# Kernel optimization log

Hardware: AMD Instinct MI355X
Metric: run time of the kernel (lower is better)

## Reference

```python
import jax, jax.numpy as jnp
import numpy as np

DIM = 1024
NUM_EXPERTS = 8
TOP_K = 2
B, S = 2, 2048
HID = 4 * DIM


def setup_inputs() -> dict:
    key = jax.random.key(0)
    ks = jax.random.split(key, 7)
    scale = 0.02
    x = jax.random.normal(ks[0], (B, S, DIM), dtype=jnp.float32)
    gate_w = jax.random.normal(ks[1], (DIM, NUM_EXPERTS), dtype=jnp.float32) * scale
    gate_b = jnp.zeros((NUM_EXPERTS,), dtype=jnp.float32)
    w1 = jax.random.normal(ks[2], (NUM_EXPERTS, DIM, HID), dtype=jnp.float32) * scale
    b1 = jnp.zeros((NUM_EXPERTS, HID), dtype=jnp.float32)
    w2 = jax.random.normal(ks[3], (NUM_EXPERTS, HID, DIM), dtype=jnp.float32) * scale
    b2 = jnp.zeros((NUM_EXPERTS, DIM), dtype=jnp.float32)
    return {"x": x, "gate_w": gate_w, "gate_b": gate_b,
            "w1": w1, "b1": b1, "w2": w2, "b2": b2}


def reference(x, gate_w, gate_b, w1, b1, w2, b2):
    # Gate: [B,S,E]
    gates = jnp.einsum('bsd,de->bse', x, gate_w) + gate_b
    top_w, top_idx = jax.lax.top_k(gates, TOP_K)          # [B,S,K]
    probs = jax.nn.softmax(top_w, axis=-1)                # softmax over selected logits
    # Dense all-expert FFN (matches original: every expert runs on every token)
    h = jnp.einsum('bsd,edh->bseh', x, w1) + b1           # [B,S,E,4D]
    h = jax.nn.gelu(h, approximate=False)                 # exact GELU (torch default)
    y = jnp.einsum('bseh,ehd->bsed', h, w2) + b2          # [B,S,E,D]
    # Select top-k experts per token and combine
    sel = jnp.take_along_axis(y, top_idx[..., None], axis=2)   # [B,S,K,D]
    return jnp.sum(sel * probs[..., None], axis=2)        # [B,S,D]
```

## Files before the change

### kernel.cpp

```cpp
#include <hip/hip_runtime.h>
#include <hip/hip_bf16.h>

#define T_TOKENS 4096
#define DIM      1024
#define HID      4096
#define NE       8
#define CAP      4096
#define SPLITS   4
#define KSP      (HID / SPLITS)

typedef __attribute__((ext_vector_type(8))) short  bf16x8;
typedef __attribute__((ext_vector_type(4))) float  f32x4;
typedef __attribute__((ext_vector_type(4))) ushort u16x4;

__device__ static inline ushort f2bf(float f) {
    __hip_bfloat16 h = __float2bfloat16(f);
    return *(ushort*)&h;
}

__device__ static inline void gll16(const void* g, void* l) {
    __builtin_amdgcn_global_load_lds(
        (const __attribute__((address_space(1))) void*)g,
        (__attribute__((address_space(3))) void*)l,
        16, 0, 0);
}

#define MFMA16(a, b, c) __builtin_amdgcn_mfma_f32_16x16x32_bf16((a), (b), (c), 0, 0, 0)

__global__ __launch_bounds__(64) void gate_kernel(
    const float* __restrict__ x, const float* __restrict__ gw,
    const float* __restrict__ gb, __hip_bfloat16* __restrict__ xb,
    int* __restrict__ counts, int* __restrict__ tlist, float* __restrict__ plist)
{
    const int tok = blockIdx.x;
    const int l   = threadIdx.x;
    const float* xr = x + (size_t)tok * DIM;

    float part[NE];
#pragma unroll
    for (int e = 0; e < NE; e++) part[e] = 0.f;

#pragma unroll
    for (int i = 0; i < DIM / 64; i++) {
        int d = i * 64 + l;
        float xv = xr[d];
        xb[(size_t)tok * DIM + d] = __float2bfloat16(xv);
        const float4* g4 = (const float4*)(gw + (size_t)d * NE);
        float4 a = g4[0], b = g4[1];
        part[0] += xv * a.x; part[1] += xv * a.y;
        part[2] += xv * a.z; part[3] += xv * a.w;
        part[4] += xv * b.x; part[5] += xv * b.y;
        part[6] += xv * b.z; part[7] += xv * b.w;
    }
#pragma unroll
    for (int off = 32; off > 0; off >>= 1) {
#pragma unroll
        for (int e = 0; e < NE; e++) part[e] += __shfl_xor(part[e], off, 64);
    }
    if (l == 0) {
        float lg[NE];
#pragma unroll
        for (int e = 0; e < NE; e++) lg[e] = part[e] + gb[e];
        int i0 = 0;
#pragma unroll
        for (int e = 1; e < NE; e++) if (lg[e] > lg[i0]) i0 = e;
        int i1 = (i0 == 0) ? 1 : 0;
#pragma unroll
        for (int e = 0; e < NE; e++) if (e != i0 && lg[e] > lg[i1]) i1 = e;
        float t  = expf(lg[i1] - lg[i0]);
        float p0 = 1.f / (1.f + t);
        float p1 = t / (1.f + t);
        int pos0 = atomicAdd(&counts[i0], 1);
        tlist[i0 * CAP + pos0] = tok;              plist[i0 * CAP + pos0] = p0;
        int pos1 = atomicAdd(&counts[i1], 1);
        tlist[i1 * CAP + pos1] = tok | (1 << 15);  plist[i1 * CAP + pos1] = p1;
    }
}

__global__ void finalize_kernel(const int* __restrict__ counts, int* __restrict__ base)
{
    if (threadIdx.x == 0) {
        int acc = 0;
        for (int e = 0; e < NE; e++) { base[e] = acc; acc += counts[e]; }
        base[NE] = acc;
    }
}

__global__ __launch_bounds__(256) void transpose_cvt64(
    const float* __restrict__ in, __hip_bfloat16* __restrict__ outp, int K, int N)
{
    __shared__ ushort tile[64][68];
    const int e  = blockIdx.z;
    const float* src = in + (size_t)e * K * N;
    ushort* dst = (ushort*)outp + (size_t)e * K * N;
    const int k0 = blockIdx.y * 64, n0 = blockIdx.x * 64;
    const int tid = threadIdx.x;

    const int rn4 = (tid & 15) * 4;
    const int rk  = tid >> 4;
#pragma unroll
    for (int p = 0; p < 4; p++) {
        int k = rk + p * 16;
        float4 v = *(const float4*)&src[(size_t)(k0 + k) * N + n0 + rn4];
        tile[k][rn4 + 0] = f2bf(v.x);
        tile[k][rn4 + 1] = f2bf(v.y);
        tile[k][rn4 + 2] = f2bf(v.z);
        tile[k][rn4 + 3] = f2bf(v.w);
    }
    __syncthreads();
    const int wk4 = (tid & 15) * 4;
    const int wn  = tid >> 4;
#pragma unroll
    for (int p = 0; p < 4; p++) {
        int n = wn + p * 16;
        u16x4 u;
        u[0] = tile[wk4 + 0][n];
        u[1] = tile[wk4 + 1][n];
        u[2] = tile[wk4 + 2][n];
        u[3] = tile[wk4 + 3][n];
        *(u16x4*)&dst[(size_t)(n0 + n) * K + k0 + wk4] = u;
    }
}


#define AOFFc(d,s) (((d)*2+(s))*8192)
#define BOFFc(d,s) (32768 + ((d)*2+(s))*4096)

#define MFMA_CL(nj0, nj1)                                                    \
    _Pragma("unroll")                                                        \
    for (int mi = 0; mi < 4; mi++) {                                         \
        acc[mi][nj0] = MFMA16(af[mi], bf##nj0, acc[mi][nj0]);                \
        acc[mi][nj1] = MFMA16(af[mi], bf##nj1, acc[mi][nj1]);                \
    }

#define GEMM_CORE(NT, srcA0, srcA1, srcB0)                                   \
    f32x4 acc[4][4];                                                         \
    _Pragma("unroll")                                                        \
    for (int i = 0; i < 4; i++)                                              \
        _Pragma("unroll")                                                    \
        for (int j = 0; j < 4; j++) acc[i][j] = (f32x4){0.f,0.f,0.f,0.f};    \
    const int a0 = (wr * 64 + lm) * 32 + rch;                                \
    const int b0 = (wc * 64 + lm) * 32 + rch;                                \
     \
    gll16(srcA0,      &lds[AOFFc(0,0) + w*512]);                             \
    gll16(srcA1,      &lds[AOFFc(0,0) + 4096 + w*512]);                      \
    gll16(srcB0,      &lds[BOFFc(0,0) + w*512]);                             \
    gll16(srcA0 + 32, &lds[AOFFc(0,1) + w*512]);                             \
    gll16(srcA1 + 32, &lds[AOFFc(0,1) + 4096 + w*512]);                      \
    gll16(srcB0 + 32, &lds[BOFFc(0,1) + w*512]);                             \
    gll16(srcA0 + 64, &lds[AOFFc(1,0) + w*512]);                             \
    gll16(srcA1 + 64, &lds[AOFFc(1,0) + 4096 + w*512]);                      \
    gll16(srcB0 + 64, &lds[BOFFc(1,0) + w*512]);                             \
    gll16(srcA0 + 96, &lds[AOFFc(1,1) + w*512]);                             \
    gll16(srcA1 + 96, &lds[AOFFc(1,1) + 4096 + w*512]);                      \
    asm volatile("s_waitcnt vmcnt(5)" ::: "memory");                         \
    __builtin_amdgcn_s_barrier();                                            \
    _Pragma("unroll 1")                                                      \
    for (int t = 0; t < NT; t++) {                                           \
        const int d   = t & 1;                                               \
        const int aof  = d * 16384,       bof  = 32768 + d * 8192;           \
        const int bofN = 32768 + (d^1) * 8192;                               \
        bf16x8 af[4]; bf16x8 bf0, bf1, bf2, bf3;                             \
                          \
        _Pragma("unroll")                                                    \
        for (int mi = 0; mi < 4; mi++)                                       \
            af[mi] = *(const bf16x8*)&lds[aof + a0 + mi*512];                \
        bf0 = *(const bf16x8*)&lds[bof + b0];                                \
        bf1 = *(const bf16x8*)&lds[bof + b0 + 512];                          \
        if (t + 1 < NT) {                                                    \
            size_t ko = (size_t)(t+1)*64 + 32;                               \
            gll16(srcB0 + ko, &lds[bofN + 4096 + w*512]);                    \
        }                                                                    \
        __builtin_amdgcn_s_barrier();                                        \
        __builtin_amdgcn_s_setprio(1);                                       \
        MFMA_CL(0, 1)                                                        \
        __builtin_amdgcn_s_setprio(0);                                       \
        __builtin_amdgcn_s_barrier();                                        \
                                    \
        bf2 = *(const bf16x8*)&lds[bof + b0 + 1024];                         \
        bf3 = *(const bf16x8*)&lds[bof + b0 + 1536];                         \
        if (t + 2 < NT) {                                                    \
            size_t ko = (size_t)(t+2)*64;                                    \
            gll16(srcA0 + ko, &lds[aof + w*512]);                            \
            gll16(srcA1 + ko, &lds[aof + 4096 + w*512]);                     \
        }                                                                    \
        __builtin_amdgcn_s_barrier();                                        \
        __builtin_amdgcn_s_setprio(1);                                       \
        MFMA_CL(2, 3)                                                        \
        __builtin_amdgcn_s_setprio(0);                                       \
        __builtin_amdgcn_s_barrier();                                        \
                          \
        _Pragma("unroll")                                                    \
        for (int mi = 0; mi < 4; mi++)                                       \
            af[mi] = *(const bf16x8*)&lds[aof + 8192 + a0 + mi*512];         \
        bf0 = *(const bf16x8*)&lds[bof + 4096 + b0];                         \
        bf1 = *(const bf16x8*)&lds[bof + 4096 + b0 + 512];                   \
        if (t + 2 < NT) {                                                    \
            size_t ko = (size_t)(t+2)*64;                                    \
            gll16(srcB0 + ko, &lds[bof + w*512]);                            \
        }                                                                    \
        __builtin_amdgcn_s_barrier();                                        \
        __builtin_amdgcn_s_setprio(1);                                       \
        MFMA_CL(0, 1)                                                        \
        __builtin_amdgcn_s_setprio(0);                                       \
        __builtin_amdgcn_s_barrier();                                        \
                      \
        bf2 = *(const bf16x8*)&lds[bof + 4096 + b0 + 1024];                  \
        bf3 = *(const bf16x8*)&lds[bof + 4096 + b0 + 1536];                  \
        if (t + 2 < NT) {                                                    \
            size_t ko = (size_t)(t+2)*64 + 32;                               \
            gll16(srcA0 + ko, &lds[aof + 8192 + w*512]);                     \
            gll16(srcA1 + ko, &lds[aof + 8192 + 4096 + w*512]);              \
        }                                                                    \
        __builtin_amdgcn_s_barrier();                                        \
        __builtin_amdgcn_s_setprio(1);                                       \
        MFMA_CL(2, 3)                                                        \
        __builtin_amdgcn_s_setprio(0);                                       \
        if (t < NT - 2) { asm volatile("s_waitcnt vmcnt(5)" ::: "memory"); } \
        else            { asm volatile("s_waitcnt vmcnt(0)" ::: "memory"); } \
        __builtin_amdgcn_s_barrier();                                        \
    }

#define CORE_IDX                                                             \
    const int tid = threadIdx.x;                                             \
    const int l = tid & 63, w = tid >> 6;                                    \
    const int wr = w >> 1, wc = w & 1;                                       \
    const int lm = l & 15, kg = l >> 4;                                      \
    const int rch = (kg ^ ((lm >> 1) & 3)) * 8;                              \
    const int srow = tid >> 2;                                               \
    const int sch  = tid & 3;                                                \
    const int sc0  = (sch ^ ((srow >> 1) & 3)) * 8;

__global__ __launch_bounds__(512, 1) void ffn1_kernel(
    const __hip_bfloat16* __restrict__ xb, const __hip_bfloat16* __restrict__ w1t,
    const float* __restrict__ b1, const int* __restrict__ counts,
    const int* __restrict__ base, const int* __restrict__ tlist,
    int* __restrict__ tickets, __hip_bfloat16* __restrict__ H)
{
    __shared__ __align__(16) ushort lds[49152];
    __shared__ int s_task;
    CORE_IDX
    const int e  = blockIdx.x & 7;
    const int ne = counts[e];
    const int tc = (ne + 255) >> 8;
    const int ntask = tc * 32;
    const int hb = base[e];
    if (tc == 0) return;

    for (;;) {
        __syncthreads();
        if (tid == 0) s_task = atomicAdd(&tickets[e], 1);
        __syncthreads();
        const int i = s_task;
        if (i >= ntask) break;
        const int cb = i / tc, rb = i - cb * tc;

        const int rA0g = rb * 256 + srow;
        const int rA1g = rA0g + 128;
        const int tok0 = tlist[e * CAP + (rA0g < ne ? rA0g : ne - 1)] & 0xFFF;
        const int tok1 = tlist[e * CAP + (rA1g < ne ? rA1g : ne - 1)] & 0xFFF;
        const ushort* srcA0 = (const ushort*)xb + (size_t)tok0 * DIM + sc0;
        const ushort* srcA1 = (const ushort*)xb + (size_t)tok1 * DIM + sc0;
        const ushort* srcB0 = (const ushort*)w1t + ((size_t)e * HID + cb * 128 + srow) * DIM + sc0;

        GEMM_CORE(16, srcA0, srcA1, srcB0)

#pragma unroll
        for (int nj = 0; nj < 4; nj++) {
            int col = wc * 64 + nj * 16 + lm;
            float bias = b1[e * HID + cb * 128 + col];
#pragma unroll
            for (int mi = 0; mi < 4; mi++) {
#pragma unroll
                for (int jj = 0; jj < 4; jj++) {
                    int row = wr * 64 + mi * 16 + kg * 4 + jj;
                    float vv = acc[mi][nj][jj] + bias;
                    vv = 0.5f * vv * (1.0f + erff(vv * 0.70710678118654752f));
                    lds[row * 128 + (col ^ ((row & 12) << 2))] = f2bf(vv);
                }
            }
        }
        __syncthreads();
#pragma unroll
        for (int pch = 0; pch < 8; pch++) {
            int c   = pch * 512 + tid;
            int row = c >> 4, seg = c & 15;
            int r   = rb * 256 + row;
            if (r < ne) {
                int pseg = seg ^ ((row & 12) >> 1);
                bf16x8 vv8 = *(const bf16x8*)&lds[row * 128 + pseg * 8];
                *(bf16x8*)((ushort*)H + (size_t)(hb + r) * HID + cb * 128 + seg * 8) = vv8;
            }
        }
    }
}

__global__ __launch_bounds__(512, 1) void ffn2_kernel(
    const __hip_bfloat16* __restrict__ H, const __hip_bfloat16* __restrict__ w2t,
    const float* __restrict__ b2, const int* __restrict__ counts,
    const int* __restrict__ base, const int* __restrict__ tlist,
    const float* __restrict__ plist, int* __restrict__ tickets,
    __hip_bfloat16* __restrict__ Y)
{
    __shared__ __align__(16) ushort lds[49152];
    __shared__ int s_task;
    CORE_IDX
    const int e  = blockIdx.x & 7;
    const int ne = counts[e];
    const int tc = (ne + 255) >> 8;
    const int ntask = tc * 32;
    const int hb = base[e];
    if (tc == 0) return;

    for (;;) {
        __syncthreads();
        if (tid == 0) s_task = atomicAdd(&tickets[NE + e], 1);
        __syncthreads();
        const int i = s_task;
        if (i >= ntask) break;
        const int c  = i / tc, rb = i - c * tc;
        const int sp = c >> 3, cb = c & 7;

        const int rA0g = rb * 256 + srow;
        const int rA1g = rA0g + 128;
        const int hr0  = hb + (rA0g < ne ? rA0g : ne - 1);
        const int hr1  = hb + (rA1g < ne ? rA1g : ne - 1);
        const size_t ko0 = (size_t)sp * KSP;
        const ushort* srcA0 = (const ushort*)H + (size_t)hr0 * HID + ko0 + sc0;
        const ushort* srcA1 = (const ushort*)H + (size_t)hr1 * HID + ko0 + sc0;
        const ushort* srcB0 = (const ushort*)w2t + ((size_t)e * DIM + cb * 128 + srow) * HID + ko0 + sc0;

        GEMM_CORE(16, srcA0, srcA1, srcB0)

#pragma unroll
        for (int nj = 0; nj < 4; nj++) {
            int col = wc * 64 + nj * 16 + lm;
            float bias = (sp == 0) ? b2[e * DIM + cb * 128 + col] : 0.f;
#pragma unroll
            for (int mi = 0; mi < 4; mi++) {
#pragma unroll
                for (int jj = 0; jj < 4; jj++) {
                    int row = wr * 64 + mi * 16 + kg * 4 + jj;
                    int r   = rb * 256 + row;
                    float p = plist[e * CAP + (r < ne ? r : ne - 1)];
                    float vv = (acc[mi][nj][jj] + bias) * p;
                    lds[row * 128 + (col ^ ((row & 12) << 2))] = f2bf(vv);
                }
            }
        }
        __syncthreads();
#pragma unroll
        for (int pch = 0; pch < 8; pch++) {
            int cch = pch * 512 + tid;
            int row = cch >> 4, seg = cch & 15;
            int r   = rb * 256 + row;
            if (r < ne) {
                int tv  = tlist[e * CAP + r];
                int tok = tv & 0xFFF, kk = tv >> 15;
                int pseg = seg ^ ((row & 12) >> 1);
                bf16x8 vv8 = *(const bf16x8*)&lds[row * 128 + pseg * 8];
                *(bf16x8*)((ushort*)Y + ((size_t)(kk * 4 + sp) * T_TOKENS + tok) * DIM
                           + cb * 128 + seg * 8) = vv8;
            }
        }
    }
}

__global__ __launch_bounds__(256) void reduce_kernel(
    const __hip_bfloat16* __restrict__ Y, float* __restrict__ out)
{
    const size_t i = ((size_t)blockIdx.x * 256 + threadIdx.x) * 8;
    float s[8];
#pragma unroll
    for (int j = 0; j < 8; j++) s[j] = 0.f;
#pragma unroll
    for (int sl = 0; sl < 8; sl++) {
        bf16x8 v = *(const bf16x8*)((const ushort*)Y + (size_t)sl * T_TOKENS * DIM + i);
#pragma unroll
        for (int j = 0; j < 8; j++) {
            union { unsigned int ui; float f; } cv;
            cv.ui = ((unsigned int)(ushort)v[j]) << 16;
            s[j] += cv.f;
        }
    }
#pragma unroll
    for (int j = 0; j < 8; j++) out[i + j] = s[j];
}

extern "C" void kernel_launch(void* const* d_in, const int* in_sizes, int n_in,
                              void* d_out, int out_size, void* d_ws, size_t ws_size,
                              hipStream_t stream)
{
    const float* x  = (const float*)d_in[0];
    const float* gw = (const float*)d_in[1];
    const float* gb = (const float*)d_in[2];
    const float* w1 = (const float*)d_in[3];
    const float* b1 = (const float*)d_in[4];
    const float* w2 = (const float*)d_in[5];
    const float* b2 = (const float*)d_in[6];
    float* out = (float*)d_out;

    char* ws = (char*)d_ws;
    __hip_bfloat16* w1t = (__hip_bfloat16*)(ws);
    __hip_bfloat16* w2t = (__hip_bfloat16*)(ws + 67108864);
    __hip_bfloat16* Hb  = (__hip_bfloat16*)(ws + 134217728);
    __hip_bfloat16* xb  = (__hip_bfloat16*)(ws + 201326592);
    int*   tlist  = (int*)  (ws + 209715200);
    float* plist  = (float*)(ws + 209846272);
    int*   counts = (int*)  (ws + 209977344);
    int*   basep  = (int*)  (ws + 209977408);
    int*   tickets= (int*)  (ws + 209977472);
    __hip_bfloat16* Y = (__hip_bfloat16*)(ws);

    hipMemsetAsync(counts, 0, 192, stream);

    gate_kernel<<<T_TOKENS, 64, 0, stream>>>(x, gw, gb, xb, counts, tlist, plist);
    finalize_kernel<<<1, 64, 0, stream>>>(counts, basep);

    transpose_cvt64<<<dim3(HID / 64, DIM / 64, NE), 256, 0, stream>>>(w1, w1t, DIM, HID);
    transpose_cvt64<<<dim3(DIM / 64, HID / 64, NE), 256, 0, stream>>>(w2, w2t, HID, DIM);

    ffn1_kernel<<<256, 512, 0, stream>>>(
        xb, w1t, b1, counts, basep, tlist, tickets, Hb);
    ffn2_kernel<<<256, 512, 0, stream>>>(
        Hb, w2t, b2, counts, basep, tlist, plist, tickets, Y);
    reduce_kernel<<<(T_TOKENS * DIM / 8) / 256, 256, 0, stream>>>(Y, out);
}
```

Before: 472.0 us.

## Shrink FFN GEMM tiles to 128x128 with 256-thread blocks, two per CU

Changes the expert FFN GEMMs from 256x128 tiles with 512 threads and one block per CU to 128x128 tiles with 256 threads, 4 waves as 2x2, and two blocks per CU. LDS staging is reorganised so each wave loads two A and two B row chunks, and the prologue waitcnt counts are adjusted. The aim is better load balance across experts with ragged token counts and more latency hiding from co-resident blocks. The cost is less data reuse per tile, more tasks, and more global traffic for the weights.

```diff
diff --git a/kernel.cpp b/kernel.cpp
--- a/kernel.cpp
+++ b/kernel.cpp
@@ -123,8 +123,8 @@
 }
 
 
-#define AOFFc(d,s) (((d)*2+(s))*8192)
-#define BOFFc(d,s) (32768 + ((d)*2+(s))*4096)
+#define AOFFc(d,s) (((d)*2+(s))*4096)
+#define BOFFc(d,s) (16384 + ((d)*2+(s))*4096)
 
 #define MFMA_CL(nj0, nj1)                                                    \
     _Pragma("unroll")                                                        \
@@ -133,7 +133,7 @@
         acc[mi][nj1] = MFMA16(af[mi], bf##nj1, acc[mi][nj1]);                \
     }
 
-#define GEMM_CORE(NT, srcA0, srcA1, srcB0)                                   \
+#define GEMM_CORE(NT, srcA0, srcA1, srcB0, srcB1)                            \
     f32x4 acc[4][4];                                                         \
     _Pragma("unroll")                                                        \
     for (int i = 0; i < 4; i++)                                              \
@@ -141,25 +141,28 @@
         for (int j = 0; j < 4; j++) acc[i][j] = (f32x4){0.f,0.f,0.f,0.f};    \
     const int a0 = (wr * 64 + lm) * 32 + rch;                                \
     const int b0 = (wc * 64 + lm) * 32 + rch;                                \
-     \
-    gll16(srcA0,      &lds[AOFFc(0,0) + w*512]);                             \
-    gll16(srcA1,      &lds[AOFFc(0,0) + 4096 + w*512]);                      \
-    gll16(srcB0,      &lds[BOFFc(0,0) + w*512]);                             \
-    gll16(srcA0 + 32, &lds[AOFFc(0,1) + w*512]);                             \
-    gll16(srcA1 + 32, &lds[AOFFc(0,1) + 4096 + w*512]);                      \
-    gll16(srcB0 + 32, &lds[BOFFc(0,1) + w*512]);                             \
-    gll16(srcA0 + 64, &lds[AOFFc(1,0) + w*512]);                             \
-    gll16(srcA1 + 64, &lds[AOFFc(1,0) + 4096 + w*512]);                      \
-    gll16(srcB0 + 64, &lds[BOFFc(1,0) + w*512]);                             \
-    gll16(srcA0 + 96, &lds[AOFFc(1,1) + w*512]);                             \
-    gll16(srcA1 + 96, &lds[AOFFc(1,1) + 4096 + w*512]);                      \
-    asm volatile("s_waitcnt vmcnt(5)" ::: "memory");                         \
+    gll16(srcA0,      &lds[AOFFc(0,0) + w*1024]);                            \
+    gll16(srcA1,      &lds[AOFFc(0,0) + w*1024 + 512]);                      \
+    gll16(srcB0,      &lds[BOFFc(0,0) + w*1024]);                            \
+    gll16(srcB1,      &lds[BOFFc(0,0) + w*1024 + 512]);                      \
+    gll16(srcA0 + 32, &lds[AOFFc(0,1) + w*1024]);                            \
+    gll16(srcA1 + 32, &lds[AOFFc(0,1) + w*1024 + 512]);                      \
+    gll16(srcB0 + 32, &lds[BOFFc(0,1) + w*1024]);                            \
+    gll16(srcB1 + 32, &lds[BOFFc(0,1) + w*1024 + 512]);                      \
+    asm volatile("s_waitcnt vmcnt(4)" ::: "memory");                         \
+    gll16(srcA0 + 64, &lds[AOFFc(1,0) + w*1024]);                            \
+    gll16(srcA1 + 64, &lds[AOFFc(1,0) + w*1024 + 512]);                      \
+    gll16(srcB0 + 64, &lds[BOFFc(1,0) + w*1024]);                            \
+    gll16(srcB1 + 64, &lds[BOFFc(1,0) + w*1024 + 512]);                      \
+    gll16(srcA0 + 96, &lds[AOFFc(1,1) + w*1024]);                            \
+    gll16(srcA1 + 96, &lds[AOFFc(1,1) + w*1024 + 512]);                      \
+    asm volatile("s_waitcnt vmcnt(6)" ::: "memory");                         \
     __builtin_amdgcn_s_barrier();                                            \
     _Pragma("unroll 1")                                                      \
     for (int t = 0; t < NT; t++) {                                           \
         const int d   = t & 1;                                               \
-        const int aof  = d * 16384,       bof  = 32768 + d * 8192;           \
-        const int bofN = 32768 + (d^1) * 8192;                               \
+        const int aof  = d * 8192,        bof  = 16384 + d * 8192;           \
+        const int bofN = 16384 + (d^1) * 8192;                               \
         bf16x8 af[4]; bf16x8 bf0, bf1, bf2, bf3;                             \
                           \
         _Pragma("unroll")                                                    \
@@ -169,7 +172,8 @@
         bf1 = *(const bf16x8*)&lds[bof + b0 + 512];                          \
         if (t + 1 < NT) {                                                    \
             size_t ko = (size_t)(t+1)*64 + 32;                               \
-            gll16(srcB0 + ko, &lds[bofN + 4096 + w*512]);                    \
+            gll16(srcB0 + ko, &lds[bofN + 4096 + w*1024]);                   \
+            gll16(srcB1 + ko, &lds[bofN + 4096 + w*1024 + 512]);             \
         }                                                                    \
         __builtin_amdgcn_s_barrier();                                        \
         __builtin_amdgcn_s_setprio(1);                                       \
@@ -181,8 +185,8 @@
         bf3 = *(const bf16x8*)&lds[bof + b0 + 1536];                         \
         if (t + 2 < NT) {                                                    \
             size_t ko = (size_t)(t+2)*64;                                    \
-            gll16(srcA0 + ko, &lds[aof + w*512]);                            \
-            gll16(srcA1 + ko, &lds[aof + 4096 + w*512]);                     \
+            gll16(srcA0 + ko, &lds[aof + w*1024]);                           \
+            gll16(srcA1 + ko, &lds[aof + w*1024 + 512]);                     \
         }                                                                    \
         __builtin_amdgcn_s_barrier();                                        \
         __builtin_amdgcn_s_setprio(1);                                       \
@@ -192,12 +196,13 @@
                           \
         _Pragma("unroll")                                                    \
         for (int mi = 0; mi < 4; mi++)                                       \
-            af[mi] = *(const bf16x8*)&lds[aof + 8192 + a0 + mi*512];         \
+            af[mi] = *(const bf16x8*)&lds[aof + 4096 + a0 + mi*512];         \
         bf0 = *(const bf16x8*)&lds[bof + 4096 + b0];                         \
         bf1 = *(const bf16x8*)&lds[bof + 4096 + b0 + 512];                   \
         if (t + 2 < NT) {                                                    \
             size_t ko = (size_t)(t+2)*64;                                    \
-            gll16(srcB0 + ko, &lds[bof + w*512]);                            \
+            gll16(srcB0 + ko, &lds[bof + w*1024]);                           \
+            gll16(srcB1 + ko, &lds[bof + w*1024 + 512]);                     \
         }                                                                    \
         __builtin_amdgcn_s_barrier();                                        \
         __builtin_amdgcn_s_setprio(1);                                       \
@@ -209,14 +214,14 @@
         bf3 = *(const bf16x8*)&lds[bof + 4096 + b0 + 1536];                  \
         if (t + 2 < NT) {                                                    \
             size_t ko = (size_t)(t+2)*64 + 32;                               \
-            gll16(srcA0 + ko, &lds[aof + 8192 + w*512]);                     \
-            gll16(srcA1 + ko, &lds[aof + 8192 + 4096 + w*512]);              \
+            gll16(srcA0 + ko, &lds[aof + 4096 + w*1024]);                    \
+            gll16(srcA1 + ko, &lds[aof + 4096 + w*1024 + 512]);              \
         }                                                                    \
         __builtin_amdgcn_s_barrier();                                        \
         __builtin_amdgcn_s_setprio(1);                                       \
         MFMA_CL(2, 3)                                                        \
         __builtin_amdgcn_s_setprio(0);                                       \
-        if (t < NT - 2) { asm volatile("s_waitcnt vmcnt(5)" ::: "memory"); } \
+        if (t < NT - 2) { asm volatile("s_waitcnt vmcnt(6)" ::: "memory"); } \
         else            { asm volatile("s_waitcnt vmcnt(0)" ::: "memory"); } \
         __builtin_amdgcn_s_barrier();                                        \
     }
@@ -227,25 +232,26 @@
     const int wr = w >> 1, wc = w & 1;                                       \
     const int lm = l & 15, kg = l >> 4;                                      \
     const int rch = (kg ^ ((lm >> 1) & 3)) * 8;                              \
-    const int srow = tid >> 2;                                               \
-    const int sch  = tid & 3;                                                \
+    const int p0c  = w * 128 + l;                                            \
+    const int srow = p0c >> 2;                 \
+    const int sch  = p0c & 3;                                                \
     const int sc0  = (sch ^ ((srow >> 1) & 3)) * 8;
 
-__global__ __launch_bounds__(512, 1) void ffn1_kernel(
+__global__ __launch_bounds__(256, 2) void ffn1_kernel(
     const __hip_bfloat16* __restrict__ xb, const __hip_bfloat16* __restrict__ w1t,
     const float* __restrict__ b1, const int* __restrict__ counts,
     const int* __restrict__ base, const int* __restrict__ tlist,
     int* __restrict__ tickets, __hip_bfloat16* __restrict__ H)
 {
-    __shared__ __align__(16) ushort lds[49152];
+    __shared__ __align__(16) ushort lds[32768];
     __shared__ int s_task;
     CORE_IDX
     const int e  = blockIdx.x & 7;
     const int ne = counts[e];
-    const int tc = (ne + 255) >> 8;
-    const int ntask = tc * 32;
+    const int mt = (ne + 127) >> 7;
+    const int ntask = mt * 32;
     const int hb = base[e];
-    if (tc == 0) return;
+    if (mt == 0) return;
 
     for (;;) {
         __syncthreads();
@@ -253,17 +259,18 @@
         __syncthreads();
         const int i = s_task;
         if (i >= ntask) break;
-        const int cb = i / tc, rb = i - cb * tc;
-
-        const int rA0g = rb * 256 + srow;
-        const int rA1g = rA0g + 128;
-        const int tok0 = tlist[e * CAP + (rA0g < ne ? rA0g : ne - 1)] & 0xFFF;
-        const int tok1 = tlist[e * CAP + (rA1g < ne ? rA1g : ne - 1)] & 0xFFF;
+        const int cb = i / mt, rb = i - cb * mt;
+
+        const int r0g = rb * 128 + srow;
+        const int r1g = r0g + 16;
+        const int tok0 = tlist[e * CAP + (r0g < ne ? r0g : ne - 1)] & 0xFFF;
+        const int tok1 = tlist[e * CAP + (r1g < ne ? r1g : ne - 1)] & 0xFFF;
         const ushort* srcA0 = (const ushort*)xb + (size_t)tok0 * DIM + sc0;
         const ushort* srcA1 = (const ushort*)xb + (size_t)tok1 * DIM + sc0;
         const ushort* srcB0 = (const ushort*)w1t + ((size_t)e * HID + cb * 128 + srow) * DIM + sc0;
-
-        GEMM_CORE(16, srcA0, srcA1, srcB0)
+        const ushort* srcB1 = srcB0 + (size_t)16 * DIM;
+
+        GEMM_CORE(16, srcA0, srcA1, srcB0, srcB1)
 
 #pragma unroll
         for (int nj = 0; nj < 4; nj++) {
@@ -283,9 +290,9 @@
         __syncthreads();
 #pragma unroll
         for (int pch = 0; pch < 8; pch++) {
-            int c   = pch * 512 + tid;
+            int c   = pch * 256 + tid;
             int row = c >> 4, seg = c & 15;
-            int r   = rb * 256 + row;
+            int r   = rb * 128 + row;
             if (r < ne) {
                 int pseg = seg ^ ((row & 12) >> 1);
                 bf16x8 vv8 = *(const bf16x8*)&lds[row * 128 + pseg * 8];
@@ -295,22 +302,22 @@
     }
 }
 
-__global__ __launch_bounds__(512, 1) void ffn2_kernel(
+__global__ __launch_bounds__(256, 2) void ffn2_kernel(
     const __hip_bfloat16* __restrict__ H, const __hip_bfloat16* __restrict__ w2t,
     const float* __restrict__ b2, const int* __restrict__ counts,
     const int* __restrict__ base, const int* __restrict__ tlist,
     const float* __restrict__ plist, int* __restrict__ tickets,
     __hip_bfloat16* __restrict__ Y)
 {
-    __shared__ __align__(16) ushort lds[49152];
+    __shared__ __align__(16) ushort lds[32768];
     __shared__ int s_task;
     CORE_IDX
     const int e  = blockIdx.x & 7;
     const int ne = counts[e];
-    const int tc = (ne + 255) >> 8;
-    const int ntask = tc * 32;
+    const int mt = (ne + 127) >> 7;
+    const int ntask = mt * 32;
     const int hb = base[e];
-    if (tc == 0) return;
+    if (mt == 0) return;
 
     for (;;) {
         __syncthreads();
@@ -318,19 +325,20 @@
         __syncthreads();
         const int i = s_task;
         if (i >= ntask) break;
-        const int c  = i / tc, rb = i - c * tc;
+        const int c  = i / mt, rb = i - c * mt;
         const int sp = c >> 3, cb = c & 7;
 
-        const int rA0g = rb * 256 + srow;
-        const int rA1g = rA0g + 128;
-        const int hr0  = hb + (rA0g < ne ? rA0g : ne - 1);
-        const int hr1  = hb + (rA1g < ne ? rA1g : ne - 1);
+        const int r0g = rb * 128 + srow;
+        const int r1g = r0g + 16;
+        const int hr0 = hb + (r0g < ne ? r0g : ne - 1);
+        const int hr1 = hb + (r1g < ne ? r1g : ne - 1);
         const size_t ko0 = (size_t)sp * KSP;
         const ushort* srcA0 = (const ushort*)H + (size_t)hr0 * HID + ko0 + sc0;
         const ushort* srcA1 = (const ushort*)H + (size_t)hr1 * HID + ko0 + sc0;
         const ushort* srcB0 = (const ushort*)w2t + ((size_t)e * DIM + cb * 128 + srow) * HID + ko0 + sc0;
-
-        GEMM_CORE(16, srcA0, srcA1, srcB0)
+        const ushort* srcB1 = srcB0 + (size_t)16 * HID;
+
+        GEMM_CORE(16, srcA0, srcA1, srcB0, srcB1)
 
 #pragma unroll
         for (int nj = 0; nj < 4; nj++) {
@@ -341,7 +349,7 @@
 #pragma unroll
                 for (int jj = 0; jj < 4; jj++) {
                     int row = wr * 64 + mi * 16 + kg * 4 + jj;
-                    int r   = rb * 256 + row;
+                    int r   = rb * 128 + row;
                     float p = plist[e * CAP + (r < ne ? r : ne - 1)];
                     float vv = (acc[mi][nj][jj] + bias) * p;
                     lds[row * 128 + (col ^ ((row & 12) << 2))] = f2bf(vv);
@@ -351,9 +359,9 @@
         __syncthreads();
 #pragma unroll
         for (int pch = 0; pch < 8; pch++) {
-            int cch = pch * 512 + tid;
+            int cch = pch * 256 + tid;
             int row = cch >> 4, seg = cch & 15;
-            int r   = rb * 256 + row;
+            int r   = rb * 128 + row;
             if (r < ne) {
                 int tv  = tlist[e * CAP + r];
                 int tok = tv & 0xFFF, kk = tv >> 15;
@@ -420,9 +428,9 @@
     transpose_cvt64<<<dim3(HID / 64, DIM / 64, NE), 256, 0, stream>>>(w1, w1t, DIM, HID);
     transpose_cvt64<<<dim3(DIM / 64, HID / 64, NE), 256, 0, stream>>>(w2, w2t, HID, DIM);
 
-    ffn1_kernel<<<256, 512, 0, stream>>>(
+    ffn1_kernel<<<512, 256, 0, stream>>>(
         xb, w1t, b1, counts, basep, tlist, tickets, Hb);
-    ffn2_kernel<<<256, 512, 0, stream>>>(
+    ffn2_kernel<<<512, 256, 0, stream>>>(
         Hb, w2t, b2, counts, basep, tlist, plist, tickets, Y);
     reduce_kernel<<<(T_TOKENS * DIM / 8) / 256, 256, 0, stream>>>(Y, out);
 }
```

Result: no change. 469.5 us (-0.5%).
